# Performance work log

Hardware: AMD Instinct MI355X
Metric: run time of the kernel (lower is better)

Reference implementation:

```python
import jax, jax.numpy as jnp
import numpy as np

MODEL_DIM = 1024
HEADS = 16
HEAD_DIM = MODEL_DIM // HEADS
OUT_DIM = 1024
B, S = 2, 2048


def setup_inputs() -> dict:
    key = jax.random.key(0)
    ks = jax.random.split(key, 10)
    scale = 1.0 / np.sqrt(MODEL_DIM)
    return {
        "query": jax.random.normal(ks[0], (B, S, MODEL_DIM), dtype=jnp.float32),
        "bank": jax.random.normal(ks[1], (B, S, MODEL_DIM), dtype=jnp.float32),
        "Wq": jax.random.normal(ks[2], (MODEL_DIM, MODEL_DIM), dtype=jnp.float32) * scale,
        "bq": jnp.zeros((MODEL_DIM,), dtype=jnp.float32),
        "Wk": jax.random.normal(ks[3], (MODEL_DIM, MODEL_DIM), dtype=jnp.float32) * scale,
        "bk": jnp.zeros((MODEL_DIM,), dtype=jnp.float32),
        "Wv": jax.random.normal(ks[4], (MODEL_DIM, MODEL_DIM), dtype=jnp.float32) * scale,
        "bv": jnp.zeros((MODEL_DIM,), dtype=jnp.float32),
        "Wo": jax.random.normal(ks[5], (OUT_DIM, MODEL_DIM), dtype=jnp.float32) * scale,
        "bo": jnp.zeros((OUT_DIM,), dtype=jnp.float32),
    }


def _split_heads(x):
    # [B, S, D] -> [B, H, S, hd]
    b, s, _ = x.shape
    return x.reshape(b, s, HEADS, HEAD_DIM).transpose(0, 2, 1, 3)


def reference(query, bank, Wq, bq, Wk, bk, Wv, bv, Wo, bo):
    # Linear projections (torch Linear: x @ W.T + b)
    q = _split_heads(query @ Wq.T + bq)  # [B,H,Sq,hd]
    k = _split_heads(bank @ Wk.T + bk)   # [B,H,Sk,hd]
    v = _split_heads(bank @ Wv.T + bv)   # [B,H,Sk,hd]
    score_scale = jnp.sqrt(jnp.float32(HEAD_DIM))
    scores = jnp.einsum("bhqd,bhkd->bhqk", q / score_scale, k)  # [B,H,Sq,Sk]
    attn = jax.nn.softmax(scores, axis=-1)
    # dropout is identity in eval-mode reference
    ctx = jnp.einsum("bhqk,bhkd->bhqd", attn, v)  # [B,H,Sq,hd]
    b, h, sq, hd = ctx.shape
    ctx = ctx.transpose(0, 2, 1, 3).reshape(b, sq, MODEL_DIM)
    return ctx @ Wo.T + bo
```

## Files before the change

kernel.cpp:

```cpp
#include <hip/hip_runtime.h>


#define BDIM   2
#define SDIM   2048
#define DDIM   1024
#define HEADS  16
#define HD     64
#define MROWS  (BDIM * SDIM)

typedef float  f32x4  __attribute__((ext_vector_type(4)));
typedef __bf16 bf16x8 __attribute__((ext_vector_type(8)));
typedef __bf16 bf16x4 __attribute__((ext_vector_type(4)));

#define QSCALE 0.18033688011112042f

__device__ __forceinline__ void stage16(const void* g, void* l) {
    __builtin_amdgcn_global_load_lds((const __attribute__((address_space(1))) void*)g,
                                     (__attribute__((address_space(3))) void*)l,
                                     16, 0, 0);
}

__global__ __launch_bounds__(256) void cvt8(const float* __restrict__ in,
                                            __bf16* __restrict__ out, int n8) {
    int i = blockIdx.x * 256 + threadIdx.x;
    if (i >= n8) return;
    const float4* p = (const float4*)in;
    float4 a = p[2 * i];
    float4 c = p[2 * i + 1];
    bf16x8 o;
    o[0] = (__bf16)a.x; o[1] = (__bf16)a.y; o[2] = (__bf16)a.z; o[3] = (__bf16)a.w;
    o[4] = (__bf16)c.x; o[5] = (__bf16)c.y; o[6] = (__bf16)c.z; o[7] = (__bf16)c.w;
    *(bf16x8*)(out + 8 * i) = o;
}

__global__ __launch_bounds__(256) void cvt8w(const float* __restrict__ w0,
                                             const float* __restrict__ w1,
                                             const float* __restrict__ w2,
                                             const float* __restrict__ w3,
                                             __bf16* __restrict__ o0,
                                             __bf16* __restrict__ o1,
                                             __bf16* __restrict__ o2,
                                             __bf16* __restrict__ o3) {
    const int sel = blockIdx.x >> 9;
    const float* in  = (sel == 0) ? w0 : (sel == 1) ? w1 : (sel == 2) ? w2 : w3;
    __bf16*      out = (sel == 0) ? o0 : (sel == 1) ? o1 : (sel == 2) ? o2 : o3;
    int i = (blockIdx.x & 511) * 256 + threadIdx.x;
    const float4* p = (const float4*)in;
    float4 a = p[2 * i];
    float4 c = p[2 * i + 1];
    bf16x8 o;
    o[0] = (__bf16)a.x; o[1] = (__bf16)a.y; o[2] = (__bf16)a.z; o[3] = (__bf16)a.w;
    o[4] = (__bf16)c.x; o[5] = (__bf16)c.y; o[6] = (__bf16)c.z; o[7] = (__bf16)c.w;
    *(bf16x8*)(out + 8 * i) = o;
}

template <bool QKV>
__global__ __launch_bounds__(256) void gemm_bt(
    const __bf16* __restrict__ Aq, const __bf16* __restrict__ Akv,
    const __bf16* __restrict__ W0, const __bf16* __restrict__ W1,
    const __bf16* __restrict__ W2,
    const float* __restrict__ b0, const float* __restrict__ b1,
    const float* __restrict__ b2,
    __bf16* __restrict__ Qo, __bf16* __restrict__ Ko, __bf16* __restrict__ Vo,
    float* __restrict__ Fo) {
    __shared__ __align__(16) __bf16 ldsA[128 * 32];
    __shared__ __align__(16) __bf16 ldsB[128 * 32];

    const int t = threadIdx.x;
    const int l = t & 63;
    const int w = t >> 6;
    const int z = QKV ? (int)blockIdx.z : 0;

    const __bf16* A  = (QKV && z != 0) ? Akv : Aq;
    const __bf16* Wm = (z == 0) ? W0 : (z == 1 ? W1 : W2);
    const float*  bias = (z == 0) ? b0 : (z == 1 ? b1 : b2);

    const int row0 = blockIdx.y * 128;
    const int col0 = blockIdx.x * 128;

    const __bf16* ga = A  + (size_t)(row0 + (t >> 2)) * DDIM + (t & 3) * 8;
    const __bf16* gb = Wm + (size_t)(col0 + (t >> 2)) * DDIM + (t & 3) * 8;
    __bf16* la = ldsA + (t & ~63) * 8;
    __bf16* lb = ldsB + (t & ~63) * 8;

    const int wm = w >> 1, wn = w & 1;
    const int aoff = (wm * 64 + (l & 15)) * 32 + (l >> 4) * 8;
    const int boff = (wn * 64 + (l & 15)) * 32 + (l >> 4) * 8;

    f32x4 acc[4][4] = {};

    for (int kb = 0; kb < DDIM; kb += 32) {
        __syncthreads();
        stage16(ga + kb,             la);
        stage16(ga + kb + 64 * DDIM, la + 2048);
        stage16(gb + kb,             lb);
        stage16(gb + kb + 64 * DDIM, lb + 2048);
        __syncthreads();

        bf16x8 af[4], bf[4];
#pragma unroll
        for (int m = 0; m < 4; ++m) af[m] = *(const bf16x8*)(ldsA + aoff + m * 16 * 32);
#pragma unroll
        for (int n = 0; n < 4; ++n) bf[n] = *(const bf16x8*)(ldsB + boff + n * 16 * 32);
#pragma unroll
        for (int m = 0; m < 4; ++m)
#pragma unroll
            for (int n = 0; n < 4; ++n)
                acc[m][n] = __builtin_amdgcn_mfma_f32_16x16x32_bf16(af[m], bf[n], acc[m][n], 0, 0, 0);
    }

#pragma unroll
    for (int m = 0; m < 4; ++m) {
        const int rbase = row0 + wm * 64 + m * 16 + (l >> 4) * 4;
#pragma unroll
        for (int n = 0; n < 4; ++n) {
            const int col = col0 + wn * 64 + n * 16 + (l & 15);
            const float bv = bias[col];
            if constexpr (QKV) {
                const int hh = col >> 6, d = col & 63;
#pragma unroll
                for (int j = 0; j < 4; ++j) {
                    const int r = rbase + j;
                    const int b = r >> 11, s = r & 2047;
                    const float v = acc[m][n][j] + bv;
                    if (z == 0) {
                        Qo[(((b * HEADS + hh) * SDIM + s) << 6) + d] = (__bf16)(v * QSCALE);
                    } else if (z == 1) {
                        Ko[(((b * HEADS + hh) * SDIM + s) << 6) + d] = (__bf16)v;
                    } else {
                        Vo[(((b * HEADS + hh) * HD + d) << 11) + s] = (__bf16)v;
                    }
                }
            } else {
#pragma unroll
                for (int j = 0; j < 4; ++j) {
                    Fo[(size_t)(rbase + j) * DDIM + col] = acc[m][n][j] + bv;
                }
            }
        }
    }
}

__global__ __launch_bounds__(512) void attn_fwd(const __bf16* __restrict__ Qb,
                                                const __bf16* __restrict__ Kb,
                                                const __bf16* __restrict__ Vtb,
                                                __bf16* __restrict__ Cb) {
    __shared__ __align__(16) __bf16 ldsK[2][2][64 * 64];
    __shared__ __align__(16) __bf16 ldsV[2][2][64 * 64];

    const int t = threadIdx.x;
    const int l = t & 63;
    const int w = t >> 6;
    const int i15 = l & 15;
    const int q4 = l >> 4;

    const int bid  = blockIdx.x;
    const int xcd  = bid & 7;
    const int wloc = bid >> 3;
    const int bh   = xcd * 4 + (wloc >> 4);
    const int qb   = wloc & 15;
    const int b    = bh >> 4;
    const int h    = bh & 15;
    const size_t base = (size_t)bh * SDIM * HD;
    const int q0 = qb * 128;

    const __bf16* qp = Qb + base + (size_t)(q0 + w * 16 + i15) * HD + q4 * 8;
    const bf16x8 qf0 = *(const bf16x8*)(qp);
    const bf16x8 qf1 = *(const bf16x8*)(qp + 32);

    const int r0 = t >> 3;
    const int sl = (t & 7) ^ (r0 & 7);
    const int sig0 = ((r0 >> 5) << 5) | (((r0 >> 2) & 3) << 3)
                   | (((r0 >> 4) & 1) << 2) | (r0 & 3);
    const __bf16* gk = Kb  + base + (size_t)sig0 * HD + sl * 8;
    const __bf16* gv = Vtb + base + (size_t)r0 * SDIM + sl * 8;
    const int wb = (t & ~63) * 8;

    const int xr = i15 & 7;
    int off[4][2];
#pragma unroll
    for (int n = 0; n < 4; ++n)
#pragma unroll
        for (int hh = 0; hh < 2; ++hh)
            off[n][hh] = (n * 16 + i15) * 64 + (((hh * 4 + q4) ^ xr) << 3);

    bf16x8 ones;
#pragma unroll
    for (int j = 0; j < 8; ++j) ones[j] = (__bf16)1.0f;

    f32x4 c[4] = {};
    f32x4 lsum = {};

    stage16(gk,           &ldsK[0][0][wb]);
    stage16(gk + 64 * HD, &ldsK[0][1][wb]);
    stage16(gv,           &ldsV[0][0][wb]);
    stage16(gv + 64,      &ldsV[0][1][wb]);

    for (int r = 0; r < SDIM / 128; ++r) {
        const int bb = r & 1;
        __syncthreads();

        if (r + 1 < SDIM / 128) {
            const int s0 = (r + 1) * 128;
            stage16(gk + (size_t)s0 * HD,        &ldsK[bb ^ 1][0][wb]);
            stage16(gk + (size_t)(s0 + 64) * HD, &ldsK[bb ^ 1][1][wb]);
            stage16(gv + s0,                     &ldsV[bb ^ 1][0][wb]);
            stage16(gv + s0 + 64,                &ldsV[bb ^ 1][1][wb]);
        }

        const __bf16* lk0 = &ldsK[bb][0][0];
        const __bf16* lk1 = &ldsK[bb][1][0];
        const __bf16* lv0 = &ldsV[bb][0][0];
        const __bf16* lv1 = &ldsV[bb][1][0];

        f32x4 sA[4] = {}, sB[4] = {};
        __builtin_amdgcn_s_setprio(1);
#pragma unroll
        for (int n = 0; n < 4; ++n) {
            bf16x8 k0 = *(const bf16x8*)(lk0 + off[n][0]);
            bf16x8 k1 = *(const bf16x8*)(lk0 + off[n][1]);
            sA[n] = __builtin_amdgcn_mfma_f32_16x16x32_bf16(k0, qf0, sA[n], 0, 0, 0);
            sA[n] = __builtin_amdgcn_mfma_f32_16x16x32_bf16(k1, qf1, sA[n], 0, 0, 0);
        }
#pragma unroll
        for (int n = 0; n < 4; ++n) {
            bf16x8 k0 = *(const bf16x8*)(lk1 + off[n][0]);
            bf16x8 k1 = *(const bf16x8*)(lk1 + off[n][1]);
            sB[n] = __builtin_amdgcn_mfma_f32_16x16x32_bf16(k0, qf0, sB[n], 0, 0, 0);
            sB[n] = __builtin_amdgcn_mfma_f32_16x16x32_bf16(k1, qf1, sB[n], 0, 0, 0);
        }
        __builtin_amdgcn_s_setprio(0);

#pragma unroll
        for (int n = 0; n < 4; ++n)
#pragma unroll
            for (int j = 0; j < 4; ++j) {
                sA[n][j] = exp2f(sA[n][j]);
                sB[n][j] = exp2f(sB[n][j]);
            }

        bf16x8 paA0, paB0, paA1, paB1;
#pragma unroll
        for (int j = 0; j < 4; ++j) {
            paA0[j]     = (__bf16)sA[0][j];
            paA0[j + 4] = (__bf16)sA[1][j];
            paB0[j]     = (__bf16)sA[2][j];
            paB0[j + 4] = (__bf16)sA[3][j];
            paA1[j]     = (__bf16)sB[0][j];
            paA1[j + 4] = (__bf16)sB[1][j];
            paB1[j]     = (__bf16)sB[2][j];
            paB1[j + 4] = (__bf16)sB[3][j];
        }

        __builtin_amdgcn_s_setprio(1);
        lsum = __builtin_amdgcn_mfma_f32_16x16x32_bf16(ones, paA0, lsum, 0, 0, 0);
        lsum = __builtin_amdgcn_mfma_f32_16x16x32_bf16(ones, paB0, lsum, 0, 0, 0);
        lsum = __builtin_amdgcn_mfma_f32_16x16x32_bf16(ones, paA1, lsum, 0, 0, 0);
        lsum = __builtin_amdgcn_mfma_f32_16x16x32_bf16(ones, paB1, lsum, 0, 0, 0);
#pragma unroll
        for (int n2 = 0; n2 < 4; ++n2) {
            bf16x8 v0 = *(const bf16x8*)(lv0 + off[n2][0]);
            bf16x8 v1 = *(const bf16x8*)(lv0 + off[n2][1]);
            c[n2] = __builtin_amdgcn_mfma_f32_16x16x32_bf16(v0, paA0, c[n2], 0, 0, 0);
            c[n2] = __builtin_amdgcn_mfma_f32_16x16x32_bf16(v1, paB0, c[n2], 0, 0, 0);
            bf16x8 u0 = *(const bf16x8*)(lv1 + off[n2][0]);
            bf16x8 u1 = *(const bf16x8*)(lv1 + off[n2][1]);
            c[n2] = __builtin_amdgcn_mfma_f32_16x16x32_bf16(u0, paA1, c[n2], 0, 0, 0);
            c[n2] = __builtin_amdgcn_mfma_f32_16x16x32_bf16(u1, paB1, c[n2], 0, 0, 0);
        }
        __builtin_amdgcn_s_setprio(0);
    }

    const float inv = 1.0f / lsum[0];
    const int q = q0 + w * 16 + i15;
#pragma unroll
    for (int n2 = 0; n2 < 4; ++n2) {
        bf16x4 o;
#pragma unroll
        for (int j = 0; j < 4; ++j) o[j] = (__bf16)(c[n2][j] * inv);
        *(bf16x4*)(Cb + (size_t)(b * SDIM + q) * DDIM + h * HD + n2 * 16 + q4 * 4) = o;
    }
}

extern "C" void kernel_launch(void* const* d_in, const int* in_sizes, int n_in,
                              void* d_out, int out_size, void* d_ws, size_t ws_size,
                              hipStream_t stream) {
    const float* query = (const float*)d_in[0];
    const float* bank  = (const float*)d_in[1];
    const float* Wq = (const float*)d_in[2];
    const float* bq = (const float*)d_in[3];
    const float* Wk = (const float*)d_in[4];
    const float* bk = (const float*)d_in[5];
    const float* Wv = (const float*)d_in[6];
    const float* bv = (const float*)d_in[7];
    const float* Wo = (const float*)d_in[8];
    const float* bo = (const float*)d_in[9];
    float* out = (float*)d_out;

    char* ws = (char*)d_ws;
    __bf16* xq  = (__bf16*)(ws);
    __bf16* xkv = (__bf16*)(ws + (8u  << 20));
    __bf16* wq  = (__bf16*)(ws + (16u << 20));
    __bf16* wk  = (__bf16*)(ws + (18u << 20));
    __bf16* wv  = (__bf16*)(ws + (20u << 20));
    __bf16* wo  = (__bf16*)(ws + (22u << 20));
    __bf16* qbuf = (__bf16*)(ws + (24u << 20));
    __bf16* kbuf = (__bf16*)(ws + (32u << 20));
    __bf16* vtbuf = (__bf16*)(ws + (40u << 20));
    __bf16* ctx = xq;

    cvt8<<<2048, 256, 0, stream>>>(query, xq, 524288);
    cvt8<<<2048, 256, 0, stream>>>(bank, xkv, 524288);
    cvt8w<<<2048, 256, 0, stream>>>(Wq, Wk, Wv, Wo, wq, wk, wv, wo);

    gemm_bt<true><<<dim3(8, 32, 3), 256, 0, stream>>>(
        xq, xkv, wq, wk, wv, bq, bk, bv, qbuf, kbuf, vtbuf, nullptr);

    attn_fwd<<<512, 512, 0, stream>>>(qbuf, kbuf, vtbuf, ctx);

    gemm_bt<false><<<dim3(8, 32, 1), 256, 0, stream>>>(
        ctx, nullptr, wo, nullptr, nullptr, bo, nullptr, nullptr,
        nullptr, nullptr, nullptr, out);
}
```

Baseline: 139.1 us.

## Merge conversion kernels, narrow output GEMM tiles, unroll attention loop

Folds the three fp32-to-bf16 conversion launches into one kernel that picks its source and destination by global thread index, which removes two launch gaps. The output projection GEMM now uses 128x64 tiles, so it launches 512 blocks instead of 256 and fills more CUs. The attention key loop is unrolled by two. The smaller tile lowers data reuse per block, and the unroll raises register pressure.

```diff
diff --git a/kernel.cpp b/kernel.cpp
--- a/kernel.cpp
+++ b/kernel.cpp
@@ -20,41 +20,36 @@
                                      16, 0, 0);
 }
 
-__global__ __launch_bounds__(256) void cvt8(const float* __restrict__ in,
-                                            __bf16* __restrict__ out, int n8) {
-    int i = blockIdx.x * 256 + threadIdx.x;
-    if (i >= n8) return;
+__global__ __launch_bounds__(256) void cvt_all(
+    const float* __restrict__ q, const float* __restrict__ bank,
+    const float* __restrict__ Wq, const float* __restrict__ Wk,
+    const float* __restrict__ Wv, const float* __restrict__ Wo,
+    __bf16* __restrict__ xq, __bf16* __restrict__ xkv,
+    __bf16* __restrict__ wq, __bf16* __restrict__ wk,
+    __bf16* __restrict__ wv, __bf16* __restrict__ wo) {
+    const int i = blockIdx.x * 256 + threadIdx.x;
+    const float* in;
+    __bf16* out;
+    int off;
+    if (i < 524288)       { in = q;    out = xq;  off = i; }
+    else if (i < 1048576) { in = bank; out = xkv; off = i - 524288; }
+    else {
+        const int j = i - 1048576;
+        const int sel = j >> 17;
+        off = j & 131071;
+        in  = (sel == 0) ? Wq : (sel == 1) ? Wk : (sel == 2) ? Wv : Wo;
+        out = (sel == 0) ? wq : (sel == 1) ? wk : (sel == 2) ? wv : wo;
+    }
     const float4* p = (const float4*)in;
-    float4 a = p[2 * i];
-    float4 c = p[2 * i + 1];
+    float4 a = p[2 * off];
+    float4 c = p[2 * off + 1];
     bf16x8 o;
     o[0] = (__bf16)a.x; o[1] = (__bf16)a.y; o[2] = (__bf16)a.z; o[3] = (__bf16)a.w;
     o[4] = (__bf16)c.x; o[5] = (__bf16)c.y; o[6] = (__bf16)c.z; o[7] = (__bf16)c.w;
-    *(bf16x8*)(out + 8 * i) = o;
-}
-
-__global__ __launch_bounds__(256) void cvt8w(const float* __restrict__ w0,
-                                             const float* __restrict__ w1,
-                                             const float* __restrict__ w2,
-                                             const float* __restrict__ w3,
-                                             __bf16* __restrict__ o0,
-                                             __bf16* __restrict__ o1,
-                                             __bf16* __restrict__ o2,
-                                             __bf16* __restrict__ o3) {
-    const int sel = blockIdx.x >> 9;
-    const float* in  = (sel == 0) ? w0 : (sel == 1) ? w1 : (sel == 2) ? w2 : w3;
-    __bf16*      out = (sel == 0) ? o0 : (sel == 1) ? o1 : (sel == 2) ? o2 : o3;
-    int i = (blockIdx.x & 511) * 256 + threadIdx.x;
-    const float4* p = (const float4*)in;
-    float4 a = p[2 * i];
-    float4 c = p[2 * i + 1];
-    bf16x8 o;
-    o[0] = (__bf16)a.x; o[1] = (__bf16)a.y; o[2] = (__bf16)a.z; o[3] = (__bf16)a.w;
-    o[4] = (__bf16)c.x; o[5] = (__bf16)c.y; o[6] = (__bf16)c.z; o[7] = (__bf16)c.w;
-    *(bf16x8*)(out + 8 * i) = o;
-}
-
-template <bool QKV>
+    *(bf16x8*)(out + 8 * off) = o;
+}
+
+template <int MODE>
 __global__ __launch_bounds__(256) void gemm_bt(
     const __bf16* __restrict__ Aq, const __bf16* __restrict__ Akv,
     const __bf16* __restrict__ W0, const __bf16* __restrict__ W1,
@@ -63,20 +58,22 @@
     const float* __restrict__ b2,
     __bf16* __restrict__ Qo, __bf16* __restrict__ Ko, __bf16* __restrict__ Vo,
     float* __restrict__ Fo) {
+    constexpr int NF = (MODE == 2) ? 2 : 4;
+    constexpr int NCOL = NF * 32;
     __shared__ __align__(16) __bf16 ldsA[128 * 32];
-    __shared__ __align__(16) __bf16 ldsB[128 * 32];
+    __shared__ __align__(16) __bf16 ldsB[(NCOL)*32];
 
     const int t = threadIdx.x;
     const int l = t & 63;
     const int w = t >> 6;
-    const int z = QKV ? (int)blockIdx.z : 0;
-
-    const __bf16* A  = (QKV && z != 0) ? Akv : Aq;
+    const int z = (MODE == 0) ? (int)blockIdx.z : 0;
+
+    const __bf16* A  = (MODE == 0 && z != 0) ? Akv : Aq;
     const __bf16* Wm = (z == 0) ? W0 : (z == 1 ? W1 : W2);
     const float*  bias = (z == 0) ? b0 : (z == 1 ? b1 : b2);
 
     const int row0 = blockIdx.y * 128;
-    const int col0 = blockIdx.x * 128;
+    const int col0 = blockIdx.x * NCOL;
 
     const __bf16* ga = A  + (size_t)(row0 + (t >> 2)) * DDIM + (t & 3) * 8;
     const __bf16* gb = Wm + (size_t)(col0 + (t >> 2)) * DDIM + (t & 3) * 8;
@@ -85,27 +82,28 @@
 
     const int wm = w >> 1, wn = w & 1;
     const int aoff = (wm * 64 + (l & 15)) * 32 + (l >> 4) * 8;
-    const int boff = (wn * 64 + (l & 15)) * 32 + (l >> 4) * 8;
-
-    f32x4 acc[4][4] = {};
+    const int boff = (wn * (NF * 16) + (l & 15)) * 32 + (l >> 4) * 8;
+
+    f32x4 acc[4][NF] = {};
 
     for (int kb = 0; kb < DDIM; kb += 32) {
         __syncthreads();
         stage16(ga + kb,             la);
         stage16(ga + kb + 64 * DDIM, la + 2048);
         stage16(gb + kb,             lb);
-        stage16(gb + kb + 64 * DDIM, lb + 2048);
+        if constexpr (MODE == 0)
+            stage16(gb + kb + 64 * DDIM, lb + 2048);
         __syncthreads();
 
-        bf16x8 af[4], bf[4];
+        bf16x8 af[4], bf[NF];
 #pragma unroll
         for (int m = 0; m < 4; ++m) af[m] = *(const bf16x8*)(ldsA + aoff + m * 16 * 32);
 #pragma unroll
-        for (int n = 0; n < 4; ++n) bf[n] = *(const bf16x8*)(ldsB + boff + n * 16 * 32);
+        for (int n = 0; n < NF; ++n) bf[n] = *(const bf16x8*)(ldsB + boff + n * 16 * 32);
 #pragma unroll
         for (int m = 0; m < 4; ++m)
 #pragma unroll
-            for (int n = 0; n < 4; ++n)
+            for (int n = 0; n < NF; ++n)
                 acc[m][n] = __builtin_amdgcn_mfma_f32_16x16x32_bf16(af[m], bf[n], acc[m][n], 0, 0, 0);
     }
 
@@ -113,10 +111,10 @@
     for (int m = 0; m < 4; ++m) {
         const int rbase = row0 + wm * 64 + m * 16 + (l >> 4) * 4;
 #pragma unroll
-        for (int n = 0; n < 4; ++n) {
-            const int col = col0 + wn * 64 + n * 16 + (l & 15);
+        for (int n = 0; n < NF; ++n) {
+            const int col = col0 + wn * (NF * 16) + n * 16 + (l & 15);
             const float bv = bias[col];
-            if constexpr (QKV) {
+            if constexpr (MODE == 0) {
                 const int hh = col >> 6, d = col & 63;
 #pragma unroll
                 for (int j = 0; j < 4; ++j) {
@@ -196,6 +194,7 @@
     stage16(gv,           &ldsV[0][0][wb]);
     stage16(gv + 64,      &ldsV[0][1][wb]);
 
+#pragma unroll 2
     for (int r = 0; r < SDIM / 128; ++r) {
         const int bb = r & 1;
         __syncthreads();
@@ -309,16 +308,15 @@
     __bf16* vtbuf = (__bf16*)(ws + (40u << 20));
     __bf16* ctx = xq;
 
-    cvt8<<<2048, 256, 0, stream>>>(query, xq, 524288);
-    cvt8<<<2048, 256, 0, stream>>>(bank, xkv, 524288);
-    cvt8w<<<2048, 256, 0, stream>>>(Wq, Wk, Wv, Wo, wq, wk, wv, wo);
-
-    gemm_bt<true><<<dim3(8, 32, 3), 256, 0, stream>>>(
+    cvt_all<<<6144, 256, 0, stream>>>(query, bank, Wq, Wk, Wv, Wo,
+                                      xq, xkv, wq, wk, wv, wo);
+
+    gemm_bt<0><<<dim3(8, 32, 3), 256, 0, stream>>>(
         xq, xkv, wq, wk, wv, bq, bk, bv, qbuf, kbuf, vtbuf, nullptr);
 
     attn_fwd<<<512, 512, 0, stream>>>(qbuf, kbuf, vtbuf, ctx);
 
-    gemm_bt<false><<<dim3(8, 32, 1), 256, 0, stream>>>(
+    gemm_bt<2><<<dim3(16, 32, 1), 256, 0, stream>>>(
         ctx, nullptr, wo, nullptr, nullptr, bo, nullptr, nullptr,
         nullptr, nullptr, nullptr, out);
 }
```

Result: faster. 128.5 us (-7.6%).
